# Performance work log

Measured on AMD Instinct MI355X. Metric: run time of the kernel, lower is better.

The kernel has to match this reference:

```python
import jax, jax.numpy as jnp
import numpy as np
from jax import lax

HIDDEN_DIM = 256


def _conv(x, w, b, stride):
    # x: [B,T,H,W,Cin], w: [1,kh,kw,Cin,Cout]
    y = lax.conv_general_dilated(
        x, w, window_strides=(1, stride, stride), padding='SAME',
        dimension_numbers=('NDHWC', 'DHWIO', 'NDHWC'))
    return y + b


def _encode(video, w1, b1, w2, b2, w3, b3):
    x = video / 255.0
    x = jax.nn.relu(_conv(x, w1, b1, 2))
    x = jax.nn.relu(_conv(x, w2, b2, 2))
    x = jax.nn.relu(_conv(x, w3, b3, 2))
    return x  # [B,T,H/8,W/8,HIDDEN_DIM]


def _sample_features(features, t_idx, y_idx, x_idx):
    # Bilinear sample features[b, t_idx, y_idx, x_idx] -> [B,N,C]
    B, T, H, W, C = features.shape
    t = jnp.clip(t_idx, 0, T - 1)
    y0 = jnp.clip(jnp.floor(y_idx).astype(jnp.int32), 0, H - 1)
    y1 = jnp.clip(y0 + 1, 0, H - 1)
    x0 = jnp.clip(jnp.floor(x_idx).astype(jnp.int32), 0, W - 1)
    x1 = jnp.clip(x0 + 1, 0, W - 1)
    wy1 = y_idx - y0.astype(features.dtype)
    wy0 = 1.0 - wy1
    wx1 = x_idx - x0.astype(features.dtype)
    wx0 = 1.0 - wx1
    bi = jnp.arange(B)[:, None]
    f00 = features[bi, t, y0, x0]
    f01 = features[bi, t, y0, x1]
    f10 = features[bi, t, y1, x0]
    f11 = features[bi, t, y1, x1]
    f0 = f00 * wx0[..., None] + f01 * wx1[..., None]
    f1 = f10 * wx0[..., None] + f11 * wx1[..., None]
    return f0 * wy0[..., None] + f1 * wy1[..., None]


def _forward(video, query_points, w1, b1, w2, b2, w3, b3):
    B, T, H, W, _ = video.shape
    N = query_points.shape[1]
    x = _encode(video, w1, b1, w2, b2, w3, b3)
    feat_H, feat_W = x.shape[2], x.shape[3]
    query_t = (query_points[:, :, 0] * (T - 1)).astype(jnp.int32)
    query_y = query_points[:, :, 1] * (feat_H - 1)
    query_x = query_points[:, :, 2] * (feat_W - 1)
    q = _sample_features(x, query_t, query_y, query_x)  # [B,N,C]
    # dense correlation volume [B,N,T,fH,fW]
    corr = jnp.einsum('bnc,bthwc->bnthw', q, x) / jnp.sqrt(jnp.float32(HIDDEN_DIM))
    probs = jax.nn.softmax(corr.reshape(B, N, T, feat_H * feat_W) * 10.0, axis=-1)
    yy, xx = jnp.meshgrid(jnp.arange(feat_H, dtype=x.dtype),
                          jnp.arange(feat_W, dtype=x.dtype), indexing='ij')
    coords_flat = jnp.stack([xx.flatten(), yy.flatten()], axis=-1)  # [fH*fW, 2]
    pred = jnp.einsum('bntk,kc->bntc', probs, coords_flat)
    pred = pred.at[..., 0].set(pred[..., 0] * (W / feat_W))
    pred = pred.at[..., 1].set(pred[..., 1] * (H / feat_H))
    occlusion = jax.nn.sigmoid(-jnp.max(corr, axis=(-2, -1)))  # [B,N,T]
    return pred, occlusion


def setup_inputs() -> dict:
    key = jax.random.key(0)
    ks = jax.random.split(key, 10)
    B, T, H, W, N = 2, 24, 256, 256, 512
    video = jax.random.uniform(ks[0], (B, T, H, W, 3), jnp.float32) * 255.0
    query_points = jax.random.uniform(ks[1], (B, N, 3), jnp.float32)
    s = 0.05
    w1 = jax.random.normal(ks[2], (1, 7, 7, 3, 64), jnp.float32) * s
    b1 = jnp.zeros((64,), jnp.float32)
    w2 = jax.random.normal(ks[3], (1, 3, 3, 64, 128), jnp.float32) * s
    b2 = jnp.zeros((128,), jnp.float32)
    w3 = jax.random.normal(ks[4], (1, 3, 3, 128, HIDDEN_DIM), jnp.float32) * s
    b3 = jnp.zeros((HIDDEN_DIM,), jnp.float32)
    return {'video': video, 'query_points': query_points,
            'w1': w1, 'b1': b1, 'w2': w2, 'b2': b2, 'w3': w3, 'b3': b3}


def reference(video, query_points, w1, b1, w2, b2, w3, b3):
    return _forward(video, query_points, w1, b1, w2, b2, w3, b3)
```

## Files before the change

kernel.cpp:

```cpp
#include <hip/hip_runtime.h>
#include <hip/hip_bf16.h>
#include <cstdint>
#include <cstddef>


typedef __attribute__((ext_vector_type(8))) short bf16x8;
typedef __attribute__((ext_vector_type(4))) float f32x4;

typedef const __attribute__((address_space(1))) void gv_t;
typedef __attribute__((address_space(3))) void sv_t;

__device__ __forceinline__ unsigned short bfr(float f) {
    return (unsigned short)(__bfloat16_as_ushort(__float2bfloat16(f)));
}

__global__ __launch_bounds__(256) void k_pad1(const float* __restrict__ video,
                                              __hip_bfloat16* __restrict__ pv)
{
    const int iy = blockIdx.x & 255;
    const int bt = blockIdx.x >> 8;
    const int ix = threadIdx.x;
    const float* src = video + ((size_t)(bt * 256 + iy) * 256 + ix) * 3;
    unsigned* dst = (unsigned*)(pv + ((size_t)(bt * 261) + iy + 2) * 1056);

    const float v0 = src[0], v1 = src[1], v2 = src[2];
    const unsigned lo = (unsigned)bfr(v0) | ((unsigned)bfr(v1) << 16);
    const unsigned hi = (unsigned)bfr(v2);
    dst[(2 + ix) * 2 + 0] = lo;
    dst[(2 + ix) * 2 + 1] = hi;
    if (ix < 2)   { dst[ix * 2] = 0u; dst[ix * 2 + 1] = 0u; }
    if (ix >= 250){ dst[(ix + 8) * 2] = 0u; dst[(ix + 8) * 2 + 1] = 0u; }
}

__global__ __launch_bounds__(256) void k_zeros(unsigned short* __restrict__ pv,
                                               unsigned short* __restrict__ c1p,
                                               unsigned short* __restrict__ c2p)
{
    const int i = blockIdx.x * 256 + threadIdx.x;
    if (i < 253440) {
        const int bt = i / 5280, rr = (i % 5280) / 1056, col = i % 1056;
        const int row = (rr < 2) ? rr : rr + 256;
        pv[(size_t)(bt * 261 + row) * 1056 + col] = 0;
    } else if (i < 1042944) {
        const int j = i - 253440, bt = j / 16448, k = j % 16448;
        size_t addr;
        if (k < 8256) { const int px = k >> 6, c = k & 63;
            addr = ((size_t)(bt * 129 + 128) * 129 + px) * 64 + c; }
        else { const int k2 = k - 8256, row = k2 >> 6, c = k2 & 63;
            addr = ((size_t)(bt * 129 + row) * 129 + 128) * 64 + c; }
        c1p[addr] = 0;
    } else {
        const int j = i - 1042944, bt = j / 16512, k = j % 16512;
        size_t addr;
        if (k < 8320) { const int px = k >> 7, c = k & 127;
            addr = ((size_t)(bt * 65 + 64) * 65 + px) * 128 + c; }
        else { const int k2 = k - 8320, row = k2 >> 7, c = k2 & 127;
            addr = ((size_t)(bt * 65 + row) * 65 + 64) * 128 + c; }
        c2p[addr] = 0;
    }
}

__global__ __launch_bounds__(256) void k_repack_all(const float* __restrict__ w1,
                                                    const float* __restrict__ w2,
                                                    const float* __restrict__ w3,
                                                    __hip_bfloat16* __restrict__ wp1,
                                                    __hip_bfloat16* __restrict__ wp2,
                                                    __hip_bfloat16* __restrict__ wp3)
{
    const int e = blockIdx.x * 256 + threadIdx.x;
    if (e < 14336) {
        const int j = e & 7, lane = (e >> 3) & 63, nt = (e >> 9) & 3, kh = e >> 11;
        const int k = ((lane >> 4) << 3) + j;
        const int kw = k >> 2, ci = k & 3;
        const int n = nt * 16 + (lane & 15);
        float v = (ci < 3 && kw < 7) ? w1[(size_t)((kh * 7 + kw) * 3 + ci) * 64 + n] : 0.f;
        wp1[e] = __float2bfloat16(v);
    } else if (e < 88064) {
        const int e2 = e - 14336;
        const int j = e2 & 7, lane = (e2 >> 3) & 63, nt = (e2 >> 9) & 7, ks = (e2 >> 12) & 1, tap = e2 >> 13;
        const int ci = ks * 32 + ((lane >> 4) << 3) + j;
        const int n  = nt * 16 + (lane & 15);
        wp2[e2] = __float2bfloat16(w2[(size_t)(tap * 64 + ci) * 128 + n]);
    } else {
        const int e3 = e - 88064;
        const int j = e3 & 7, lane = (e3 >> 3) & 63, nt = (e3 >> 9) & 15, ks = (e3 >> 13) & 3, tap = e3 >> 15;
        const int ci = ks * 32 + ((lane >> 4) << 3) + j;
        const int n  = nt * 16 + (lane & 15);
        wp3[e3] = __float2bfloat16(w3[(size_t)(tap * 128 + ci) * 256 + n]);
    }
}

__global__ __launch_bounds__(256) void k_conv1m(const __hip_bfloat16* __restrict__ pv,
                                                const __hip_bfloat16* __restrict__ wp,
                                                const float* __restrict__ b1,
                                                __hip_bfloat16* __restrict__ out)
{
    const int xcd = blockIdx.x & 7;
    const int sub = blockIdx.x >> 3;
    const int bt  = xcd * 6 + (sub >> 7);
    const int oy  = sub & 127;
    const int w  = threadIdx.x >> 6;
    const int l  = threadIdx.x & 63;
    const int li = l & 15, lh = l >> 4;

    f32x4 acc[2][4];
#pragma unroll
    for (int m = 0; m < 2; ++m)
#pragma unroll
        for (int n = 0; n < 4; ++n) acc[m][n] = (f32x4){0.f, 0.f, 0.f, 0.f};

    const short* pvS = (const short*)pv;
    const short* wS  = (const short*)wp;

#pragma unroll
    for (int kh = 0; kh < 7; ++kh) {
        const short* row = pvS + (size_t)(bt * 261 + oy * 2 + kh) * 1056;
        bf16x8 bw[4];
#pragma unroll
        for (int nt = 0; nt < 4; ++nt)
            bw[nt] = *reinterpret_cast<const bf16x8*>(wS + ((size_t)(kh * 4 + nt) * 64 + l) * 8);
#pragma unroll
        for (int mt = 0; mt < 2; ++mt) {
            const int ox = w * 32 + mt * 16 + li;
            bf16x8 a = *reinterpret_cast<const bf16x8*>(row + 8 * (ox + lh));
#pragma unroll
            for (int nt = 0; nt < 4; ++nt)
                acc[mt][nt] = __builtin_amdgcn_mfma_f32_16x16x32_bf16(a, bw[nt], acc[mt][nt], 0, 0, 0);
        }
    }

    __hip_bfloat16* op = out + ((size_t)(bt * 129 + oy) * 129) * 64;
#pragma unroll
    for (int mt = 0; mt < 2; ++mt) {
        const int px0 = w * 32 + mt * 16 + lh * 4;
#pragma unroll
        for (int nt = 0; nt < 4; ++nt) {
            const int n = nt * 16 + li;
            const float bias = b1[n];
#pragma unroll
            for (int r = 0; r < 4; ++r) {
                const float v = fmaxf(acc[mt][nt][r] * (1.f / 255.f) + bias, 0.f);
                op[(size_t)(px0 + r) * 64 + n] = __float2bfloat16(v);
            }
        }
    }
}

template<int CIN, int COUT, int OW, int IW, int ORS>
__global__ __launch_bounds__(256, 3) void k_convg(const __hip_bfloat16* __restrict__ in,
                                                  const __hip_bfloat16* __restrict__ wp,
                                                  const float* __restrict__ bias,
                                                  __hip_bfloat16* __restrict__ out)
{
    constexpr int KSN = CIN / 32;
    constexpr int NSL = 9 * KSN;
    constexpr int NTT = COUT / 16;
    constexpr int XT  = OW / 16;
    constexpr int RPB = 128 / OW;
    constexpr int MTB = (OW * OW) / 128;
    constexpr int NH  = COUT / 128;
    constexpr int PARTS = MTB * NH;

    __shared__ char lbuf[3][16384];

    const int bid  = blockIdx.x;
    const int xcd  = bid & 7;
    const int sub  = bid >> 3;
    const int grp  = sub / PARTS;
    const int part = sub % PARTS;
    const int bt   = xcd * 6 + grp;
    const int mblk = part % MTB;
    const int nh   = part / MTB;

    const int tid = threadIdx.x;
    const int w   = tid >> 6;
    const int l   = tid & 63;
    const int li  = l & 15, lh = l >> 4;

    const int oy0  = mblk * RPB;
    const int roy0 = oy0 * 2;

    const short* inS = (const short*)in + (size_t)bt * IW * IW * CIN;
    const char*  wB  = (const char*)wp + (size_t)(nh * 8) * 1024;

    const int g0 = tid, g1 = tid + 256;
    const int q0 = g0 >> 7, px0_ = g0 & 127;
    const int q1 = g1 >> 7, px1_ = g1 & 127;
    const short* aA0 = inS + ((size_t)(roy0 + ((px0_ >> 4) / XT) * 2) * IW
                              + ((px0_ >> 4) % XT) * 32 + (px0_ & 15) * 2) * CIN + q0 * 8;
    const short* aA1 = inS + ((size_t)(roy0 + ((px1_ >> 4) / XT) * 2) * IW
                              + ((px1_ >> 4) % XT) * 32 + (px1_ & 15) * 2) * CIN + q1 * 8;

    f32x4 acc[8][2];
#pragma unroll
    for (int mt = 0; mt < 8; ++mt) {
        acc[mt][0] = (f32x4){0.f, 0.f, 0.f, 0.f};
        acc[mt][1] = (f32x4){0.f, 0.f, 0.f, 0.f};
    }

    auto stage = [&](int S, int B) {
        const int tap = S / KSN, ks = S % KSN;
        const int kh = tap / 3, kw = tap % 3;
        const int ao = (kh * IW + kw) * CIN + ks * 32;
        char* dst = &lbuf[B][0];
        __builtin_amdgcn_global_load_lds((gv_t*)(aA0 + ao), (sv_t*)(dst + g0 * 16), 16, 0, 0);
        __builtin_amdgcn_global_load_lds((gv_t*)(aA1 + ao), (sv_t*)(dst + g1 * 16), 16, 0, 0);
        const char* bs = wB + (size_t)S * (NTT * 1024) + tid * 16;
        __builtin_amdgcn_global_load_lds((gv_t*)(bs),        (sv_t*)(dst + 8192 + tid * 16), 16, 0, 0);
        __builtin_amdgcn_global_load_lds((gv_t*)(bs + 4096), (sv_t*)(dst + 12288 + tid * 16), 16, 0, 0);
    };

    stage(0, 0);
    stage(1, 1);
    asm volatile("s_waitcnt vmcnt(4)" ::: "memory");
    __builtin_amdgcn_sched_barrier(0);
    __builtin_amdgcn_s_barrier();
    __builtin_amdgcn_sched_barrier(0);

#pragma unroll
    for (int s = 0; s < NSL; ++s) {
        if (s + 2 < NSL) stage(s + 2, (s + 2) % 3);

        const char* bufc = &lbuf[s % 3][0];
        bf16x8 af[8];
#pragma unroll
        for (int mt = 0; mt < 8; ++mt)
            af[mt] = *reinterpret_cast<const bf16x8*>(bufc + lh * 2048 + mt * 256 + li * 16);
        const bf16x8 b0 = *reinterpret_cast<const bf16x8*>(bufc + 8192 + (w * 2 + 0) * 1024 + l * 16);
        const bf16x8 b1 = *reinterpret_cast<const bf16x8*>(bufc + 8192 + (w * 2 + 1) * 1024 + l * 16);

#pragma unroll
        for (int mt = 0; mt < 8; ++mt) {
            acc[mt][0] = __builtin_amdgcn_mfma_f32_16x16x32_bf16(af[mt], b0, acc[mt][0], 0, 0, 0);
            acc[mt][1] = __builtin_amdgcn_mfma_f32_16x16x32_bf16(af[mt], b1, acc[mt][1], 0, 0, 0);
        }

        if (s + 1 < NSL) {
            if (s + 2 < NSL) asm volatile("s_waitcnt vmcnt(4)" ::: "memory");
            else             asm volatile("s_waitcnt vmcnt(0)" ::: "memory");
            __builtin_amdgcn_sched_barrier(0);
            __builtin_amdgcn_s_barrier();
            __builtin_amdgcn_sched_barrier(0);
        }
    }

    __hip_bfloat16* ob = out + (size_t)bt * ORS * ORS * COUT;
#pragma unroll
    for (int mt = 0; mt < 8; ++mt) {
        const int oy  = oy0 + mt / XT;
        const int oxb = (mt % XT) * 16 + lh * 4;
#pragma unroll
        for (int j = 0; j < 2; ++j) {
            const int n = (nh * 8 + w * 2 + j) * 16 + li;
            const float bv = bias[n];
#pragma unroll
            for (int r = 0; r < 4; ++r) {
                const float v = fmaxf(acc[mt][j][r] + bv, 0.f);
                ob[((size_t)oy * ORS + oxb + r) * COUT + n] = __float2bfloat16(v);
            }
        }
    }
}

__global__ __launch_bounds__(256) void k_sample(const float* __restrict__ qp,
                                                const __hip_bfloat16* __restrict__ feat,
                                                __hip_bfloat16* __restrict__ q)
{
    const int bn = blockIdx.x;
    const int b  = bn >> 9;
    const float t3 = qp[bn * 3 + 0];
    const float yv = qp[bn * 3 + 1] * 31.f;
    const float xv = qp[bn * 3 + 2] * 31.f;
    int t = (int)(t3 * 23.f);
    t = min(max(t, 0), 23);
    int y0 = (int)floorf(yv); y0 = min(max(y0, 0), 31);
    const int y1 = min(y0 + 1, 31);
    int x0 = (int)floorf(xv); x0 = min(max(x0, 0), 31);
    const int x1 = min(x0 + 1, 31);
    const float wy1 = yv - (float)y0, wy0 = 1.f - wy1;
    const float wx1 = xv - (float)x0, wx0 = 1.f - wx1;

    const int c = threadIdx.x;
    const __hip_bfloat16* fb = feat + ((size_t)(b * 24 + t) * 1024) * 256;
    const float f00 = __bfloat162float(fb[(size_t)(y0 * 32 + x0) * 256 + c]);
    const float f01 = __bfloat162float(fb[(size_t)(y0 * 32 + x1) * 256 + c]);
    const float f10 = __bfloat162float(fb[(size_t)(y1 * 32 + x0) * 256 + c]);
    const float f11 = __bfloat162float(fb[(size_t)(y1 * 32 + x1) * 256 + c]);
    const float v = (f00 * wx0 + f01 * wx1) * wy0 + (f10 * wx0 + f11 * wx1) * wy1;
    q[(size_t)bn * 256 + c] = __float2bfloat16(v);
}

__global__ __launch_bounds__(256, 2) void k_corrm(const __hip_bfloat16* __restrict__ qb,
                                                  const __hip_bfloat16* __restrict__ featb,
                                                  float* __restrict__ pbuf)
{
    __shared__ short lbuf[2][8192];

    const int bid = blockIdx.x;
    const int xcd = bid & 7;
    const int sub = bid >> 3;
    const int grp = sub >> 5;
    const int prt = sub & 31;
    const int img = xcd * 6 + grp;
    const int bq  = img / 24, t = img % 24;
    const int nc  = prt & 3, ps = prt >> 2;

    const int tid = threadIdx.x;
    const int w   = tid >> 6;
    const int l   = tid & 63;
    const int li  = l & 15, lh = l >> 4;

    const short* qS = (const short*)qb;
    const short* fS = (const short*)featb + (size_t)img * 1024 * 256;
    const char*  tile0 = (const char*)(fS + (size_t)(ps * 128) * 256);

    const int q0 = nc * 128 + w * 32;
    bf16x8 aq[2][8];
#pragma unroll
    for (int mt = 0; mt < 2; ++mt)
#pragma unroll
        for (int ks = 0; ks < 8; ++ks)
            aq[mt][ks] = *reinterpret_cast<const bf16x8*>(
                qS + ((size_t)(bq * 512 + q0 + mt * 16 + li)) * 256 + ks * 32 + lh * 8);

    float m[2][4], s[2][4], sx[2][4], sy[2][4], dmx[2][4];
#pragma unroll
    for (int mt = 0; mt < 2; ++mt)
#pragma unroll
        for (int r = 0; r < 4; ++r) {
            m[mt][r] = -1e30f; s[mt][r] = 0.f; sx[mt][r] = 0.f; sy[mt][r] = 0.f; dmx[mt][r] = -1e30f;
        }

    bf16x8 stg[4];
#pragma unroll
    for (int i = 0; i < 4; ++i) {
        const int g = i * 256 + tid;
        const int pos = g >> 5, kb = (g & 31) * 16;
        stg[i] = *reinterpret_cast<const bf16x8*>(tile0 + (size_t)pos * 512 + kb);
    }
#pragma unroll
    for (int i = 0; i < 4; ++i) {
        const int g = i * 256 + tid;
        const int pos = g >> 5, kb = (g & 31) * 16;
        *reinterpret_cast<bf16x8*>((char*)&lbuf[0][0] + pos * 512 + (kb ^ ((pos & 7) << 4))) = stg[i];
    }
    __syncthreads();

#pragma unroll
    for (int st = 0; st < 4; ++st) {
        const int cur = st & 1;

        if (st < 3) {
            const char* tn = tile0 + (size_t)((st + 1) * 32) * 512;
#pragma unroll
            for (int i = 0; i < 4; ++i) {
                const int g = i * 256 + tid;
                const int pos = g >> 5, kb = (g & 31) * 16;
                stg[i] = *reinterpret_cast<const bf16x8*>(tn + (size_t)pos * 512 + kb);
            }
        }

        f32x4 acc[2][2];
#pragma unroll
        for (int mt = 0; mt < 2; ++mt)
#pragma unroll
            for (int pt = 0; pt < 2; ++pt) acc[mt][pt] = (f32x4){0.f, 0.f, 0.f, 0.f};

#pragma unroll
        for (int pt = 0; pt < 2; ++pt) {
            const int p = pt * 16 + li;
#pragma unroll
            for (int ks = 0; ks < 8; ++ks) {
                const int k = ks * 32 + lh * 8;
                bf16x8 bv = *reinterpret_cast<const bf16x8*>(&lbuf[cur][p * 256 + (k ^ ((p & 7) << 3))]);
                acc[0][pt] = __builtin_amdgcn_mfma_f32_16x16x32_bf16(aq[0][ks], bv, acc[0][pt], 0, 0, 0);
                acc[1][pt] = __builtin_amdgcn_mfma_f32_16x16x32_bf16(aq[1][ks], bv, acc[1][pt], 0, 0, 0);
            }
        }

        const float py = (float)(ps * 4 + st);
#pragma unroll
        for (int mt = 0; mt < 2; ++mt)
#pragma unroll
            for (int r = 0; r < 4; ++r) {
                const float v0 = acc[mt][0][r], v1 = acc[mt][1][r];
                float mx = fmaxf(v0, v1);
                mx = fmaxf(mx, __shfl_xor(mx, 1));
                mx = fmaxf(mx, __shfl_xor(mx, 2));
                mx = fmaxf(mx, __shfl_xor(mx, 4));
                mx = fmaxf(mx, __shfl_xor(mx, 8));
                dmx[mt][r] = fmaxf(dmx[mt][r], mx);
                const float mn = fmaxf(m[mt][r], mx * 0.625f);
                const float sc = __expf(m[mt][r] - mn);
                const float e0 = __expf(v0 * 0.625f - mn);
                const float e1 = __expf(v1 * 0.625f - mn);
                const float es = e0 + e1;
                s[mt][r]  = s[mt][r]  * sc + es;
                sx[mt][r] = sx[mt][r] * sc + es * (float)li + 16.f * e1;
                sy[mt][r] = sy[mt][r] * sc + es * py;
                m[mt][r] = mn;
            }

        if (st < 3) {
#pragma unroll
            for (int i = 0; i < 4; ++i) {
                const int g = i * 256 + tid;
                const int pos = g >> 5, kb = (g & 31) * 16;
                *reinterpret_cast<bf16x8*>((char*)&lbuf[cur ^ 1][0] + pos * 512 + (kb ^ ((pos & 7) << 4))) = stg[i];
            }
            __syncthreads();
        }
    }

#pragma unroll
    for (int mt = 0; mt < 2; ++mt)
#pragma unroll
        for (int r = 0; r < 4; ++r) {
#pragma unroll
            for (int off = 1; off < 16; off <<= 1) {
                s[mt][r]  += __shfl_xor(s[mt][r],  off);
                sx[mt][r] += __shfl_xor(sx[mt][r], off);
                sy[mt][r] += __shfl_xor(sy[mt][r], off);
            }
        }

    if (li == 0) {
#pragma unroll
        for (int mt = 0; mt < 2; ++mt)
#pragma unroll
            for (int r = 0; r < 4; ++r) {
                const int n = q0 + mt * 16 + lh * 4 + r;
                const int bnt = (bq * 512 + n) * 24 + t;
                const int pi = ps * 24576 + bnt;
                pbuf[pi]                = m[mt][r];
                pbuf[196608 + pi]       = s[mt][r];
                pbuf[393216 + pi]       = sx[mt][r];
                pbuf[589824 + pi]       = sy[mt][r];
                pbuf[786432 + pi]       = dmx[mt][r];
            }
    }
}

__global__ __launch_bounds__(256) void k_merge(const float* __restrict__ pbuf,
                                               float* __restrict__ outp)
{
    const int i = blockIdx.x * 256 + threadIdx.x;
    float M = -1e30f, D = -1e30f;
#pragma unroll
    for (int ps = 0; ps < 8; ++ps) {
        M = fmaxf(M, pbuf[ps * 24576 + i]);
        D = fmaxf(D, pbuf[786432 + ps * 24576 + i]);
    }
    float s = 0.f, sx = 0.f, sy = 0.f;
#pragma unroll
    for (int ps = 0; ps < 8; ++ps) {
        const int pi = ps * 24576 + i;
        const float wgt = __expf(pbuf[pi] - M);
        s  += pbuf[196608 + pi] * wgt;
        sx += pbuf[393216 + pi] * wgt;
        sy += pbuf[589824 + pi] * wgt;
    }
    const float inv = 8.f / s;
    outp[i * 2 + 0] = sx * inv;
    outp[i * 2 + 1] = sy * inv;
    outp[49152 + i] = 1.f / (1.f + __expf(D * 0.0625f));
}

extern "C" void kernel_launch(void* const* d_in, const int* in_sizes, int n_in,
                              void* d_out, int out_size, void* d_ws, size_t ws_size,
                              hipStream_t stream)
{
    const float* video = (const float*)d_in[0];
    const float* qp    = (const float*)d_in[1];
    const float* w1    = (const float*)d_in[2];
    const float* b1    = (const float*)d_in[3];
    const float* w2    = (const float*)d_in[4];
    const float* b2    = (const float*)d_in[5];
    const float* w3    = (const float*)d_in[6];
    const float* b3    = (const float*)d_in[7];
    float* out = (float*)d_out;

    char* wsb = (char*)d_ws;
    __hip_bfloat16* c1p   = (__hip_bfloat16*)(wsb);
    __hip_bfloat16* c2p   = (__hip_bfloat16*)(wsb + 102242304ull);
    __hip_bfloat16* pv    = (__hip_bfloat16*)(wsb + 154159104ull);
    __hip_bfloat16* featb = (__hip_bfloat16*)(wsb + 154159104ull);
    __hip_bfloat16* qbuf  = (__hip_bfloat16*)(wsb + 180618240ull);
    __hip_bfloat16* w1p   = (__hip_bfloat16*)(wsb + 181142528ull);
    __hip_bfloat16* w2p   = (__hip_bfloat16*)(wsb + 181171200ull);
    __hip_bfloat16* w3p   = (__hip_bfloat16*)(wsb + 181318656ull);
    float*          pbuf  = (float*)(wsb + 181908480ull);

    k_repack_all<<<dim3(1496),     dim3(256), 0, stream>>>(w1, w2, w3, w1p, w2p, w3p);
    k_pad1      <<<dim3(48 * 256), dim3(256), 0, stream>>>(video, pv);
    k_zeros     <<<dim3(7170),     dim3(256), 0, stream>>>(
                       (unsigned short*)pv, (unsigned short*)c1p, (unsigned short*)c2p);
    k_conv1m    <<<dim3(48 * 128), dim3(256), 0, stream>>>(pv, w1p, b1, c1p);
    k_convg<64, 128, 64, 129, 65><<<dim3(1536), dim3(256), 0, stream>>>(c1p, w2p, b2, c2p);
    k_convg<128, 256, 32, 65, 32><<<dim3(768),  dim3(256), 0, stream>>>(c2p, w3p, b3, featb);
    k_sample    <<<dim3(1024),     dim3(256), 0, stream>>>(qp, featb, qbuf);
    k_corrm     <<<dim3(1536),     dim3(256), 0, stream>>>(qbuf, featb, pbuf);
    k_merge     <<<dim3(96),       dim3(256), 0, stream>>>(pbuf, out);
}
```

Baseline: 203.2 us.

## Fuse prep kernels into one launch and retile convg warps as 2x2

Three preprocessing kernels (weight repack, video pad/convert, border zeroing) are merged into a single launch dispatched by block index, which removes two kernel launches. In the generic conv kernel the per-wave tiling changes from 8 M-tiles by 2 N-tiles to a 2x2 wave grid where each wave does 4 M-tiles by 4 N-tiles. Each wave now loads 8 LDS fragments per step instead of 10 for the same 16 MFMAs. The accumulator count stays the same, so register pressure should be roughly unchanged.

```diff
diff --git a/kernel.cpp b/kernel.cpp
--- a/kernel.cpp
+++ b/kernel.cpp
@@ -14,79 +14,77 @@
     return (unsigned short)(__bfloat16_as_ushort(__float2bfloat16(f)));
 }
 
-__global__ __launch_bounds__(256) void k_pad1(const float* __restrict__ video,
-                                              __hip_bfloat16* __restrict__ pv)
-{
-    const int iy = blockIdx.x & 255;
-    const int bt = blockIdx.x >> 8;
-    const int ix = threadIdx.x;
-    const float* src = video + ((size_t)(bt * 256 + iy) * 256 + ix) * 3;
-    unsigned* dst = (unsigned*)(pv + ((size_t)(bt * 261) + iy + 2) * 1056);
-
-    const float v0 = src[0], v1 = src[1], v2 = src[2];
-    const unsigned lo = (unsigned)bfr(v0) | ((unsigned)bfr(v1) << 16);
-    const unsigned hi = (unsigned)bfr(v2);
-    dst[(2 + ix) * 2 + 0] = lo;
-    dst[(2 + ix) * 2 + 1] = hi;
-    if (ix < 2)   { dst[ix * 2] = 0u; dst[ix * 2 + 1] = 0u; }
-    if (ix >= 250){ dst[(ix + 8) * 2] = 0u; dst[(ix + 8) * 2 + 1] = 0u; }
-}
-
-__global__ __launch_bounds__(256) void k_zeros(unsigned short* __restrict__ pv,
-                                               unsigned short* __restrict__ c1p,
-                                               unsigned short* __restrict__ c2p)
-{
-    const int i = blockIdx.x * 256 + threadIdx.x;
-    if (i < 253440) {
-        const int bt = i / 5280, rr = (i % 5280) / 1056, col = i % 1056;
-        const int row = (rr < 2) ? rr : rr + 256;
-        pv[(size_t)(bt * 261 + row) * 1056 + col] = 0;
-    } else if (i < 1042944) {
-        const int j = i - 253440, bt = j / 16448, k = j % 16448;
-        size_t addr;
-        if (k < 8256) { const int px = k >> 6, c = k & 63;
-            addr = ((size_t)(bt * 129 + 128) * 129 + px) * 64 + c; }
-        else { const int k2 = k - 8256, row = k2 >> 6, c = k2 & 63;
-            addr = ((size_t)(bt * 129 + row) * 129 + 128) * 64 + c; }
-        c1p[addr] = 0;
+__global__ __launch_bounds__(256) void k_prep(const float* __restrict__ video,
+                                              const float* __restrict__ w1,
+                                              const float* __restrict__ w2,
+                                              const float* __restrict__ w3,
+                                              __hip_bfloat16* __restrict__ pv,
+                                              unsigned short* __restrict__ c1p,
+                                              unsigned short* __restrict__ c2p,
+                                              __hip_bfloat16* __restrict__ wp1,
+                                              __hip_bfloat16* __restrict__ wp2,
+                                              __hip_bfloat16* __restrict__ wp3)
+{
+    const int bid = blockIdx.x;
+    if (bid < 12288) {
+        const int iy = bid & 255;
+        const int bt = bid >> 8;
+        const int ix = threadIdx.x;
+        const float* src = video + ((size_t)(bt * 256 + iy) * 256 + ix) * 3;
+        unsigned* dst = (unsigned*)(pv + ((size_t)(bt * 261) + iy + 2) * 1056);
+        const float v0 = src[0], v1 = src[1], v2 = src[2];
+        const unsigned lo = (unsigned)bfr(v0) | ((unsigned)bfr(v1) << 16);
+        const unsigned hi = (unsigned)bfr(v2);
+        dst[(2 + ix) * 2 + 0] = lo;
+        dst[(2 + ix) * 2 + 1] = hi;
+        if (ix < 2)   { dst[ix * 2] = 0u; dst[ix * 2 + 1] = 0u; }
+        if (ix >= 250){ dst[(ix + 8) * 2] = 0u; dst[(ix + 8) * 2 + 1] = 0u; }
+    } else if (bid < 12288 + 7170) {
+        const int i = (bid - 12288) * 256 + threadIdx.x;
+        unsigned short* pvs = (unsigned short*)pv;
+        if (i < 253440) {
+            const int bt = i / 5280, rr = (i % 5280) / 1056, col = i % 1056;
+            const int row = (rr < 2) ? rr : rr + 256;
+            pvs[(size_t)(bt * 261 + row) * 1056 + col] = 0;
+        } else if (i < 1042944) {
+            const int j = i - 253440, bt = j / 16448, k = j % 16448;
+            size_t addr;
+            if (k < 8256) { const int px = k >> 6, c = k & 63;
+                addr = ((size_t)(bt * 129 + 128) * 129 + px) * 64 + c; }
+            else { const int k2 = k - 8256, row = k2 >> 6, c = k2 & 63;
+                addr = ((size_t)(bt * 129 + row) * 129 + 128) * 64 + c; }
+            c1p[addr] = 0;
+        } else if (i < 1835520) {
+            const int j = i - 1042944, bt = j / 16512, k = j % 16512;
+            size_t addr;
+            if (k < 8320) { const int px = k >> 7, c = k & 127;
+                addr = ((size_t)(bt * 65 + 64) * 65 + px) * 128 + c; }
+            else { const int k2 = k - 8320, row = k2 >> 7, c = k2 & 127;
+                addr = ((size_t)(bt * 65 + row) * 65 + 64) * 128 + c; }
+            c2p[addr] = 0;
+        }
     } else {
-        const int j = i - 1042944, bt = j / 16512, k = j % 16512;
-        size_t addr;
-        if (k < 8320) { const int px = k >> 7, c = k & 127;
-            addr = ((size_t)(bt * 65 + 64) * 65 + px) * 128 + c; }
-        else { const int k2 = k - 8320, row = k2 >> 7, c = k2 & 127;
-            addr = ((size_t)(bt * 65 + row) * 65 + 64) * 128 + c; }
-        c2p[addr] = 0;
-    }
-}
-
-__global__ __launch_bounds__(256) void k_repack_all(const float* __restrict__ w1,
-                                                    const float* __restrict__ w2,
-                                                    const float* __restrict__ w3,
-                                                    __hip_bfloat16* __restrict__ wp1,
-                                                    __hip_bfloat16* __restrict__ wp2,
-                                                    __hip_bfloat16* __restrict__ wp3)
-{
-    const int e = blockIdx.x * 256 + threadIdx.x;
-    if (e < 14336) {
-        const int j = e & 7, lane = (e >> 3) & 63, nt = (e >> 9) & 3, kh = e >> 11;
-        const int k = ((lane >> 4) << 3) + j;
-        const int kw = k >> 2, ci = k & 3;
-        const int n = nt * 16 + (lane & 15);
-        float v = (ci < 3 && kw < 7) ? w1[(size_t)((kh * 7 + kw) * 3 + ci) * 64 + n] : 0.f;
-        wp1[e] = __float2bfloat16(v);
-    } else if (e < 88064) {
-        const int e2 = e - 14336;
-        const int j = e2 & 7, lane = (e2 >> 3) & 63, nt = (e2 >> 9) & 7, ks = (e2 >> 12) & 1, tap = e2 >> 13;
-        const int ci = ks * 32 + ((lane >> 4) << 3) + j;
-        const int n  = nt * 16 + (lane & 15);
-        wp2[e2] = __float2bfloat16(w2[(size_t)(tap * 64 + ci) * 128 + n]);
-    } else {
-        const int e3 = e - 88064;
-        const int j = e3 & 7, lane = (e3 >> 3) & 63, nt = (e3 >> 9) & 15, ks = (e3 >> 13) & 3, tap = e3 >> 15;
-        const int ci = ks * 32 + ((lane >> 4) << 3) + j;
-        const int n  = nt * 16 + (lane & 15);
-        wp3[e3] = __float2bfloat16(w3[(size_t)(tap * 128 + ci) * 256 + n]);
+        const int e = (bid - 12288 - 7170) * 256 + threadIdx.x;
+        if (e < 14336) {
+            const int j = e & 7, lane = (e >> 3) & 63, nt = (e >> 9) & 3, kh = e >> 11;
+            const int k = ((lane >> 4) << 3) + j;
+            const int kw = k >> 2, ci = k & 3;
+            const int n = nt * 16 + (lane & 15);
+            float v = (ci < 3 && kw < 7) ? w1[(size_t)((kh * 7 + kw) * 3 + ci) * 64 + n] : 0.f;
+            wp1[e] = __float2bfloat16(v);
+        } else if (e < 88064) {
+            const int e2 = e - 14336;
+            const int j = e2 & 7, lane = (e2 >> 3) & 63, nt = (e2 >> 9) & 7, ks = (e2 >> 12) & 1, tap = e2 >> 13;
+            const int ci = ks * 32 + ((lane >> 4) << 3) + j;
+            const int n  = nt * 16 + (lane & 15);
+            wp2[e2] = __float2bfloat16(w2[(size_t)(tap * 64 + ci) * 128 + n]);
+        } else {
+            const int e3 = e - 88064;
+            const int j = e3 & 7, lane = (e3 >> 3) & 63, nt = (e3 >> 9) & 15, ks = (e3 >> 13) & 3, tap = e3 >> 15;
+            const int ci = ks * 32 + ((lane >> 4) << 3) + j;
+            const int n  = nt * 16 + (lane & 15);
+            wp3[e3] = __float2bfloat16(w3[(size_t)(tap * 128 + ci) * 256 + n]);
+        }
     }
 }
 
@@ -176,6 +174,7 @@
     const int w   = tid >> 6;
     const int l   = tid & 63;
     const int li  = l & 15, lh = l >> 4;
+    const int mw  = w >> 1, nw = w & 1;
 
     const int oy0  = mblk * RPB;
     const int roy0 = oy0 * 2;
@@ -191,12 +190,11 @@
     const short* aA1 = inS + ((size_t)(roy0 + ((px1_ >> 4) / XT) * 2) * IW
                               + ((px1_ >> 4) % XT) * 32 + (px1_ & 15) * 2) * CIN + q1 * 8;
 
-    f32x4 acc[8][2];
-#pragma unroll
-    for (int mt = 0; mt < 8; ++mt) {
-        acc[mt][0] = (f32x4){0.f, 0.f, 0.f, 0.f};
-        acc[mt][1] = (f32x4){0.f, 0.f, 0.f, 0.f};
-    }
+    f32x4 acc[4][4];
+#pragma unroll
+    for (int i = 0; i < 4; ++i)
+#pragma unroll
+        for (int j = 0; j < 4; ++j) acc[i][j] = (f32x4){0.f, 0.f, 0.f, 0.f};
 
     auto stage = [&](int S, int B) {
         const int tap = S / KSN, ks = S % KSN;
@@ -222,18 +220,19 @@
         if (s + 2 < NSL) stage(s + 2, (s + 2) % 3);
 
         const char* bufc = &lbuf[s % 3][0];
-        bf16x8 af[8];
-#pragma unroll
-        for (int mt = 0; mt < 8; ++mt)
-            af[mt] = *reinterpret_cast<const bf16x8*>(bufc + lh * 2048 + mt * 256 + li * 16);
-        const bf16x8 b0 = *reinterpret_cast<const bf16x8*>(bufc + 8192 + (w * 2 + 0) * 1024 + l * 16);
-        const bf16x8 b1 = *reinterpret_cast<const bf16x8*>(bufc + 8192 + (w * 2 + 1) * 1024 + l * 16);
-
-#pragma unroll
-        for (int mt = 0; mt < 8; ++mt) {
-            acc[mt][0] = __builtin_amdgcn_mfma_f32_16x16x32_bf16(af[mt], b0, acc[mt][0], 0, 0, 0);
-            acc[mt][1] = __builtin_amdgcn_mfma_f32_16x16x32_bf16(af[mt], b1, acc[mt][1], 0, 0, 0);
-        }
+        bf16x8 af[4], bf[4];
+#pragma unroll
+        for (int i = 0; i < 4; ++i)
+            af[i] = *reinterpret_cast<const bf16x8*>(bufc + lh * 2048 + (mw * 4 + i) * 256 + li * 16);
+#pragma unroll
+        for (int j = 0; j < 4; ++j)
+            bf[j] = *reinterpret_cast<const bf16x8*>(bufc + 8192 + (nw * 4 + j) * 1024 + l * 16);
+
+#pragma unroll
+        for (int i = 0; i < 4; ++i)
+#pragma unroll
+            for (int j = 0; j < 4; ++j)
+                acc[i][j] = __builtin_amdgcn_mfma_f32_16x16x32_bf16(af[i], bf[j], acc[i][j], 0, 0, 0);
 
         if (s + 1 < NSL) {
             if (s + 2 < NSL) asm volatile("s_waitcnt vmcnt(4)" ::: "memory");
@@ -246,16 +245,17 @@
 
     __hip_bfloat16* ob = out + (size_t)bt * ORS * ORS * COUT;
 #pragma unroll
-    for (int mt = 0; mt < 8; ++mt) {
+    for (int i = 0; i < 4; ++i) {
+        const int mt  = mw * 4 + i;
         const int oy  = oy0 + mt / XT;
         const int oxb = (mt % XT) * 16 + lh * 4;
 #pragma unroll
-        for (int j = 0; j < 2; ++j) {
-            const int n = (nh * 8 + w * 2 + j) * 16 + li;
+        for (int j = 0; j < 4; ++j) {
+            const int n = (nh * 8 + nw * 4 + j) * 16 + li;
             const float bv = bias[n];
 #pragma unroll
             for (int r = 0; r < 4; ++r) {
-                const float v = fmaxf(acc[mt][j][r] + bv, 0.f);
+                const float v = fmaxf(acc[i][j][r] + bv, 0.f);
                 ob[((size_t)oy * ORS + oxb + r) * COUT + n] = __float2bfloat16(v);
             }
         }
@@ -491,10 +491,9 @@
     __hip_bfloat16* w3p   = (__hip_bfloat16*)(wsb + 181318656ull);
     float*          pbuf  = (float*)(wsb + 181908480ull);
 
-    k_repack_all<<<dim3(1496),     dim3(256), 0, stream>>>(w1, w2, w3, w1p, w2p, w3p);
-    k_pad1      <<<dim3(48 * 256), dim3(256), 0, stream>>>(video, pv);
-    k_zeros     <<<dim3(7170),     dim3(256), 0, stream>>>(
-                       (unsigned short*)pv, (unsigned short*)c1p, (unsigned short*)c2p);
+    k_prep      <<<dim3(20954),    dim3(256), 0, stream>>>(
+                       video, w1, w2, w3, pv,
+                       (unsigned short*)c1p, (unsigned short*)c2p, w1p, w2p, w3p);
     k_conv1m    <<<dim3(48 * 128), dim3(256), 0, stream>>>(pv, w1p, b1, c1p);
     k_convg<64, 128, 64, 129, 65><<<dim3(1536), dim3(256), 0, stream>>>(c1p, w2p, b2, c2p);
     k_convg<128, 256, 32, 65, 32><<<dim3(768),  dim3(256), 0, stream>>>(c2p, w3p, b3, featb);
```

Result: faster. 197.0 us (-3.1%).
